# Optimization experiments

Measured on AMD Instinct MI355X. Metric: run time of the kernel, lower is better.

The kernel has to match this reference:

```python
import jax, jax.numpy as jnp
import numpy as np

B, NT, ND, NB = 2, 1024, 512, 6
K_IN, NH, K_LAT = 4 * NB + 5, 196, 128  # k_in = 2*NB*(1+1) + 2*(1+1) + 1 with USE_VELOCITIES=True
EPS_FREE = True  # norms divide exactly as in torch (no eps), randn inputs are safe


def setup_inputs() -> dict:
    key = jax.random.key(0)
    ks = jax.random.split(key, 12)
    def lin(k, fin, fout):
        kw, kb = jax.random.split(k)
        W = jax.random.normal(kw, (fin, fout), jnp.float32) / np.sqrt(fin)
        b = jax.random.normal(kb, (fout,), jnp.float32) * 0.01
        return W, b
    W0, b0 = lin(ks[0], K_IN, NH)
    W1, b1 = lin(ks[1], NH, NH)
    W2, b2 = lin(ks[2], NH, K_LAT)
    return {
        "x0": jax.random.normal(ks[3], (B, NT, 3), jnp.float32),
        "x": jax.random.normal(ks[4], (B, NT, ND, 3), jnp.float32),
        "N": jax.random.uniform(ks[5], (B, NT), jnp.float32),
        "basis": jax.random.normal(ks[6], (B, NB, 3), jnp.float32),
        "v": jax.random.normal(ks[7], (B, NT, ND, 3), jnp.float32),
        "W0": W0, "b0": b0, "W1": W1, "b1": b1, "W2": W2, "b2": b2,
    }


def _create_scalars(x0, x, N, basis, v):
    # shapes: x0 [b,i,3], x/v [b,i,j,3], N [b,i], basis [b,k,3]
    nd = x.shape[2]
    vbulk = jnp.mean(v, axis=2)                      # [b,i,3]
    vc = v - vbulk[:, :, None, :]                    # [b,i,j,3]

    bcast = lambda t: jnp.broadcast_to(t[:, :, None, :], t.shape[:2] + (nd, t.shape[-1]))

    x0n = jnp.linalg.norm(x0, axis=-1, keepdims=True)          # [b,i,1]
    x0b = jnp.einsum('bid,bkd->bik', x0 / x0n, basis)          # [b,i,NB]
    vbn = jnp.linalg.norm(vbulk, axis=-1, keepdims=True)       # [b,i,1]
    vbb = jnp.einsum('bid,bkd->bik', vbulk / vbn, basis)       # [b,i,NB]
    xn = jnp.linalg.norm(x, axis=-1, keepdims=True)            # [b,i,j,1]
    xb = jnp.einsum('bijd,bkd->bijk', x / xn, basis)           # [b,i,j,NB]
    vn = jnp.linalg.norm(vc, axis=-1, keepdims=True)           # [b,i,j,1]
    vb = jnp.einsum('bijd,bkd->bijk', vc / vn, basis)          # [b,i,j,NB]

    return jnp.concatenate([
        bcast(N[..., None]),   # N            [1]
        bcast(x0n),            # |x0|         [1]
        bcast(x0b),            # x0.basis     [NB]
        bcast(vbn),            # |vbulk|      [1]
        bcast(vbb),            # vbulk.basis  [NB]
        xn,                    # |x|          [1]
        xb,                    # x.basis      [NB]
        vn,                    # |v|          [1]
        vb,                    # v.basis      [NB]
    ], axis=-1)                # [b,i,j,K_IN]


def reference(x0, x, N, basis, v, W0, b0, W1, b1, W2, b2):
    s = _create_scalars(x0, x, N, basis, v)                    # [b,i,j,K_IN]
    h = jax.nn.leaky_relu(jnp.einsum('bijf,fh->bijh', s, W0) + b0)
    h = jnp.mean(h, axis=2)                                    # pool over N_DM -> [b,i,NH]
    h = jax.nn.leaky_relu(h @ W1 + b1)
    return h @ W2 + b2                                         # [b,i,K_LAT]
```

## Files before the change

### kernel.cpp

```cpp
#include <hip/hip_runtime.h>

typedef __bf16 bf16x8 __attribute__((ext_vector_type(8)));
typedef float f32x16 __attribute__((ext_vector_type(16)));

constexpr int NT = 1024;
constexpr int ND = 512;
constexpr int NB = 6;
constexpr int NH = 196;
constexpr int KL = 128;
constexpr int NHP = 224;

__device__ __forceinline__ unsigned short f2bf(float f) {
    unsigned int b = __float_as_uint(f);
    b += 0x7FFFu + ((b >> 16) & 1u);
    return (unsigned short)(b >> 16);
}

__global__ __launch_bounds__(448) void prep_kernel(const float* __restrict__ W0,
                                                   uint4* __restrict__ frag)
{
    const int tid = threadIdx.x;
    const int l = tid & 63;
    const int nt = tid >> 6;
    const int col = l & 31;
    const int khalf = l >> 5;
    const int c = nt * 32 + col;
    unsigned int w[4];
    #pragma unroll
    for (int d = 0; d < 4; d++) {
        int k0 = khalf * 8 + 2 * d;
        int k1 = k0 + 1;
        float v0 = (c < NH && k0 < 14) ? W0[(15 + k0) * NH + c] : 0.f;
        float v1 = (c < NH && k1 < 14) ? W0[(15 + k1) * NH + c] : 0.f;
        w[d] = (unsigned int)f2bf(v0) | ((unsigned int)f2bf(v1) << 16);
    }
    frag[tid] = make_uint4(w[0], w[1], w[2], w[3]);
}

__global__ __launch_bounds__(256) void pool_kernel(
    const float* __restrict__ x0, const float* __restrict__ x,
    const float* __restrict__ Nn, const float* __restrict__ basis,
    const float* __restrict__ v,  const float* __restrict__ W0,
    const float* __restrict__ b0, const uint4* __restrict__ w0frag,
    float* __restrict__ pool_out)
{
    __shared__ __align__(16) unsigned short featB[ND][16];
    __shared__ float consthL[NHP];
    __shared__ float pool4A[4][NHP];
    __shared__ float pool4B[4][NHP];
    __shared__ float red[4][3];

    const int r = blockIdx.x;
    const int t = threadIdx.x;
    const int wid = t >> 6;
    const int lane = t & 63;
    const int b = r >> 10;
    const size_t rowbase = (size_t)r * ND * 3;

    float s0 = 0.f, s1 = 0.f, s2 = 0.f;
    for (int j = t; j < ND; j += 256) {
        const float* vp = v + rowbase + 3 * j;
        s0 += vp[0]; s1 += vp[1]; s2 += vp[2];
    }
    #pragma unroll
    for (int off = 32; off > 0; off >>= 1) {
        s0 += __shfl_down(s0, off);
        s1 += __shfl_down(s1, off);
        s2 += __shfl_down(s2, off);
    }
    if (lane == 0) { red[wid][0] = s0; red[wid][1] = s1; red[wid][2] = s2; }
    __syncthreads();
    const float inv_nd = 1.0f / (float)ND;
    const float vb0 = (red[0][0] + red[1][0] + red[2][0] + red[3][0]) * inv_nd;
    const float vb1 = (red[0][1] + red[1][1] + red[2][1] + red[3][1]) * inv_nd;
    const float vb2 = (red[0][2] + red[1][2] + red[2][2] + red[3][2]) * inv_nd;

    float bx[NB], by[NB], bz[NB];
    {
        const float* bp = basis + (size_t)b * NB * 3;
        #pragma unroll
        for (int k = 0; k < NB; k++) { bx[k] = bp[3*k]; by[k] = bp[3*k+1]; bz[k] = bp[3*k+2]; }
    }

    for (int j = t; j < ND; j += 256) {
        const float* xp = x + rowbase + 3 * j;
        const float* vp = v + rowbase + 3 * j;
        float xa = xp[0], xbv = xp[1], xc = xp[2];
        float va = vp[0] - vb0, vbv = vp[1] - vb1, vcv = vp[2] - vb2;
        float n2x = xa*xa + xbv*xbv + xc*xc;
        float n2v = va*va + vbv*vbv + vcv*vcv;
        float rx = __frsqrt_rn(n2x);
        float rv = __frsqrt_rn(n2v);
        float f[14];
        f[0] = n2x * rx;
        #pragma unroll
        for (int k = 0; k < NB; k++) f[1+k] = (xa*bx[k] + xbv*by[k] + xc*bz[k]) * rx;
        f[7] = n2v * rv;
        #pragma unroll
        for (int k = 0; k < NB; k++) f[8+k] = (va*bx[k] + vbv*by[k] + vcv*bz[k]) * rv;
        bf16x8 lo, hi;
        #pragma unroll
        for (int e = 0; e < 8; e++) lo[e] = (__bf16)f[e];
        #pragma unroll
        for (int e = 0; e < 6; e++) hi[e] = (__bf16)f[8+e];
        hi[6] = (__bf16)0.f; hi[7] = (__bf16)0.f;
        *reinterpret_cast<uint4*>(&featB[j][0]) = __builtin_bit_cast(uint4, lo);
        *reinterpret_cast<uint4*>(&featB[j][8]) = __builtin_bit_cast(uint4, hi);
    }

    bf16x8 bfr[7];
    #pragma unroll
    for (int nt = 0; nt < 7; nt++)
        bfr[nt] = __builtin_bit_cast(bf16x8, w0frag[nt * 64 + lane]);

    float cf[15];
    {
        const float* xp = x0 + (size_t)r * 3;
        float a0 = xp[0], a1 = xp[1], a2 = xp[2];
        float n20 = a0*a0 + a1*a1 + a2*a2;
        float n2b = vb0*vb0 + vb1*vb1 + vb2*vb2;
        float r0 = __frsqrt_rn(n20);
        float r1 = __frsqrt_rn(n2b);
        cf[0] = Nn[r];
        cf[1] = n20 * r0;
        #pragma unroll
        for (int k = 0; k < NB; k++) cf[2+k] = (a0*bx[k] + a1*by[k] + a2*bz[k]) * r0;
        cf[8] = n2b * r1;
        #pragma unroll
        for (int k = 0; k < NB; k++) cf[9+k] = (vb0*bx[k] + vb1*by[k] + vb2*bz[k]) * r1;
    }
    if (t < NHP) {
        float ch = 0.f;
        if (t < NH) {
            ch = b0[t];
            #pragma unroll
            for (int f2 = 0; f2 < 15; f2++) ch += cf[f2] * W0[f2 * NH + t];
        }
        consthL[t] = ch;
    }
    __syncthreads();

    const int col = lane & 31;
    const int khalf = lane >> 5;
    float ch[7];
    #pragma unroll
    for (int nt = 0; nt < 7; nt++) ch[nt] = consthL[nt * 32 + col];

    float pA[7] = {0.f,0.f,0.f,0.f,0.f,0.f,0.f};
    float pB[7] = {0.f,0.f,0.f,0.f,0.f,0.f,0.f};
    #pragma unroll
    for (int mi = 0; mi < 4; mi++) {
        const int row = (wid * 4 + mi) * 32 + col;
        uint4 araw = *reinterpret_cast<const uint4*>(&featB[row][khalf * 8]);
        bf16x8 afrag = __builtin_bit_cast(bf16x8, araw);
        #pragma unroll
        for (int nt = 0; nt < 7; nt++) {
            f32x16 acc;
            #pragma unroll
            for (int i = 0; i < 16; i++) acc[i] = ch[nt];
            acc = __builtin_amdgcn_mfma_f32_32x32x16_bf16(afrag, bfr[nt], acc, 0, 0, 0);
            #pragma unroll
            for (int i = 0; i < 16; i++) {
                pA[nt] += acc[i];
                pB[nt] += __builtin_fabsf(acc[i]);
            }
        }
    }
    #pragma unroll
    for (int nt = 0; nt < 7; nt++) {
        pA[nt] += __shfl_xor(pA[nt], 32);
        pB[nt] += __shfl_xor(pB[nt], 32);
    }
    if (lane < 32) {
        #pragma unroll
        for (int nt = 0; nt < 7; nt++) {
            pool4A[wid][nt * 32 + lane] = pA[nt];
            pool4B[wid][nt * 32 + lane] = pB[nt];
        }
    }
    __syncthreads();

    if (t < NH) {
        float sa = pool4A[0][t] + pool4A[1][t] + pool4A[2][t] + pool4A[3][t];
        float sb = pool4B[0][t] + pool4B[1][t] + pool4B[2][t] + pool4B[3][t];
        pool_out[(size_t)r * NH + t] = (0.505f * sa + 0.495f * sb) * inv_nd;
    }
}

__global__ __launch_bounds__(256) void head_kernel(
    const float* __restrict__ pool, const float* __restrict__ W1,
    const float* __restrict__ b1,   const float* __restrict__ W2,
    const float* __restrict__ b2,   float* __restrict__ out)
{
    __shared__ __align__(16) float poolL[4][200];
    __shared__ __align__(16) float h1L[4][200];
    const int t = threadIdx.x;
    const int r0 = blockIdx.x * 4;

    if (t < NH) {
        #pragma unroll
        for (int rr = 0; rr < 4; rr++) poolL[rr][t] = pool[(size_t)(r0 + rr) * NH + t];
    }
    __syncthreads();

    if (t < NH) {
        float a0 = b1[t], a1 = b1[t], a2 = b1[t], a3 = b1[t];
        const float* wc = W1 + t;
        #pragma unroll 2
        for (int k = 0; k < NH; k += 4) {
            float w0 = wc[(size_t)(k + 0) * NH];
            float w1 = wc[(size_t)(k + 1) * NH];
            float w2 = wc[(size_t)(k + 2) * NH];
            float w3 = wc[(size_t)(k + 3) * NH];
            float4 p0 = *reinterpret_cast<const float4*>(&poolL[0][k]);
            float4 p1 = *reinterpret_cast<const float4*>(&poolL[1][k]);
            float4 p2 = *reinterpret_cast<const float4*>(&poolL[2][k]);
            float4 p3 = *reinterpret_cast<const float4*>(&poolL[3][k]);
            a0 += p0.x * w0 + p0.y * w1 + p0.z * w2 + p0.w * w3;
            a1 += p1.x * w0 + p1.y * w1 + p1.z * w2 + p1.w * w3;
            a2 += p2.x * w0 + p2.y * w1 + p2.z * w2 + p2.w * w3;
            a3 += p3.x * w0 + p3.y * w1 + p3.z * w2 + p3.w * w3;
        }
        h1L[0][t] = fmaxf(a0, 0.01f * a0);
        h1L[1][t] = fmaxf(a1, 0.01f * a1);
        h1L[2][t] = fmaxf(a2, 0.01f * a2);
        h1L[3][t] = fmaxf(a3, 0.01f * a3);
    }
    __syncthreads();

    if (t < KL) {
        float a0 = b2[t], a1 = b2[t], a2 = b2[t], a3 = b2[t];
        const float* wc = W2 + t;
        #pragma unroll 2
        for (int k = 0; k < NH; k += 4) {
            float w0 = wc[(size_t)(k + 0) * KL];
            float w1 = wc[(size_t)(k + 1) * KL];
            float w2 = wc[(size_t)(k + 2) * KL];
            float w3 = wc[(size_t)(k + 3) * KL];
            float4 p0 = *reinterpret_cast<const float4*>(&h1L[0][k]);
            float4 p1 = *reinterpret_cast<const float4*>(&h1L[1][k]);
            float4 p2 = *reinterpret_cast<const float4*>(&h1L[2][k]);
            float4 p3 = *reinterpret_cast<const float4*>(&h1L[3][k]);
            a0 += p0.x * w0 + p0.y * w1 + p0.z * w2 + p0.w * w3;
            a1 += p1.x * w0 + p1.y * w1 + p1.z * w2 + p1.w * w3;
            a2 += p2.x * w0 + p2.y * w1 + p2.z * w2 + p2.w * w3;
            a3 += p3.x * w0 + p3.y * w1 + p3.z * w2 + p3.w * w3;
        }
        out[(size_t)(r0 + 0) * KL + t] = a0;
        out[(size_t)(r0 + 1) * KL + t] = a1;
        out[(size_t)(r0 + 2) * KL + t] = a2;
        out[(size_t)(r0 + 3) * KL + t] = a3;
    }
}

extern "C" void kernel_launch(void* const* d_in, const int* in_sizes, int n_in,
                              void* d_out, int out_size, void* d_ws, size_t ws_size,
                              hipStream_t stream) {
    const float* x0    = (const float*)d_in[0];
    const float* x     = (const float*)d_in[1];
    const float* Nn    = (const float*)d_in[2];
    const float* basis = (const float*)d_in[3];
    const float* v     = (const float*)d_in[4];
    const float* W0    = (const float*)d_in[5];
    const float* b0    = (const float*)d_in[6];
    const float* W1    = (const float*)d_in[7];
    const float* b1    = (const float*)d_in[8];
    const float* W2    = (const float*)d_in[9];
    const float* b2    = (const float*)d_in[10];
    float* out = (float*)d_out;

    const int rows = in_sizes[2];
    float* pool_ws = (float*)d_ws;
    uint4* w0frag  = (uint4*)((char*)d_ws + (size_t)rows * NH * 4);

    prep_kernel<<<dim3(1), dim3(448), 0, stream>>>(W0, w0frag);
    pool_kernel<<<dim3(rows), dim3(256), 0, stream>>>(
        x0, x, Nn, basis, v, W0, b0, w0frag, pool_ws);
    head_kernel<<<dim3(rows / 4), dim3(256), 0, stream>>>(
        pool_ws, W1, b1, W2, b2, out);
}
```

Measured before the change: 151.4 us.

## Move head MLP layers to bf16 MFMA kernels with pre-packed weight fragments

```diff
diff --git a/kernel.cpp b/kernel.cpp
--- a/kernel.cpp
+++ b/kernel.cpp
@@ -9,6 +9,12 @@
 constexpr int NH = 196;
 constexpr int KL = 128;
 constexpr int NHP = 224;
+constexpr int KP = 208;
+
+constexpr size_t W0F_OFF = 0;
+constexpr size_t W1F_OFF = 7168;
+constexpr size_t W2F_OFF = 100352;
+constexpr size_t H1B_OFF = 153600;
 
 __device__ __forceinline__ unsigned short f2bf(float f) {
     unsigned int b = __float_as_uint(f);
@@ -16,25 +22,56 @@
     return (unsigned short)(b >> 16);
 }
 
-__global__ __launch_bounds__(448) void prep_kernel(const float* __restrict__ W0,
-                                                   uint4* __restrict__ frag)
+__global__ __launch_bounds__(256) void prep_kernel(
+    const float* __restrict__ W0, const float* __restrict__ W1,
+    const float* __restrict__ W2,
+    uint4* __restrict__ w0f, uint4* __restrict__ w1f, uint4* __restrict__ w2f)
 {
-    const int tid = threadIdx.x;
-    const int l = tid & 63;
-    const int nt = tid >> 6;
-    const int col = l & 31;
-    const int khalf = l >> 5;
-    const int c = nt * 32 + col;
-    unsigned int w[4];
-    #pragma unroll
-    for (int d = 0; d < 4; d++) {
-        int k0 = khalf * 8 + 2 * d;
-        int k1 = k0 + 1;
-        float v0 = (c < NH && k0 < 14) ? W0[(15 + k0) * NH + c] : 0.f;
-        float v1 = (c < NH && k1 < 14) ? W0[(15 + k1) * NH + c] : 0.f;
-        w[d] = (unsigned int)f2bf(v0) | ((unsigned int)f2bf(v1) << 16);
-    }
-    frag[tid] = make_uint4(w[0], w[1], w[2], w[3]);
+    const int tid = blockIdx.x * 256 + threadIdx.x;
+    if (tid < 448) {
+        const int l = tid & 63, nt = tid >> 6;
+        const int c = nt * 32 + (l & 31);
+        const int khalf = l >> 5;
+        unsigned int w[4];
+        #pragma unroll
+        for (int d = 0; d < 4; d++) {
+            int k0 = khalf * 8 + 2 * d, k1 = k0 + 1;
+            float v0 = (c < NH && k0 < 14) ? W0[(15 + k0) * NH + c] : 0.f;
+            float v1 = (c < NH && k1 < 14) ? W0[(15 + k1) * NH + c] : 0.f;
+            w[d] = (unsigned int)f2bf(v0) | ((unsigned int)f2bf(v1) << 16);
+        }
+        w0f[tid] = make_uint4(w[0], w[1], w[2], w[3]);
+    } else if (tid < 448 + 7 * 13 * 64) {
+        const int i = tid - 448;
+        const int l = i & 63, rest = i >> 6;
+        const int ks = rest % 13, nt = rest / 13;
+        const int c = nt * 32 + (l & 31);
+        const int kb = ks * 16 + (l >> 5) * 8;
+        unsigned int w[4];
+        #pragma unroll
+        for (int d = 0; d < 4; d++) {
+            int k0 = kb + 2 * d, k1 = k0 + 1;
+            float v0 = (c < NH && k0 < NH) ? W1[(size_t)k0 * NH + c] : 0.f;
+            float v1 = (c < NH && k1 < NH) ? W1[(size_t)k1 * NH + c] : 0.f;
+            w[d] = (unsigned int)f2bf(v0) | ((unsigned int)f2bf(v1) << 16);
+        }
+        w1f[i] = make_uint4(w[0], w[1], w[2], w[3]);
+    } else if (tid < 448 + 7 * 13 * 64 + 4 * 13 * 64) {
+        const int i = tid - 448 - 7 * 13 * 64;
+        const int l = i & 63, rest = i >> 6;
+        const int ks = rest % 13, nt = rest / 13;
+        const int c = nt * 32 + (l & 31);
+        const int kb = ks * 16 + (l >> 5) * 8;
+        unsigned int w[4];
+        #pragma unroll
+        for (int d = 0; d < 4; d++) {
+            int k0 = kb + 2 * d, k1 = k0 + 1;
+            float v0 = (k0 < NH) ? W2[(size_t)k0 * KL + c] : 0.f;
+            float v1 = (k1 < NH) ? W2[(size_t)k1 * KL + c] : 0.f;
+            w[d] = (unsigned int)f2bf(v0) | ((unsigned int)f2bf(v1) << 16);
+        }
+        w2f[i] = make_uint4(w[0], w[1], w[2], w[3]);
+    }
 }
 
 __global__ __launch_bounds__(256) void pool_kernel(
@@ -42,7 +79,7 @@
     const float* __restrict__ Nn, const float* __restrict__ basis,
     const float* __restrict__ v,  const float* __restrict__ W0,
     const float* __restrict__ b0, const uint4* __restrict__ w0frag,
-    float* __restrict__ pool_out)
+    unsigned short* __restrict__ pool_out)
 {
     __shared__ __align__(16) unsigned short featB[ND][16];
     __shared__ float consthL[NHP];
@@ -180,76 +217,78 @@
     }
     __syncthreads();
 
-    if (t < NH) {
-        float sa = pool4A[0][t] + pool4A[1][t] + pool4A[2][t] + pool4A[3][t];
-        float sb = pool4B[0][t] + pool4B[1][t] + pool4B[2][t] + pool4B[3][t];
-        pool_out[(size_t)r * NH + t] = (0.505f * sa + 0.495f * sb) * inv_nd;
-    }
-}
-
-__global__ __launch_bounds__(256) void head_kernel(
-    const float* __restrict__ pool, const float* __restrict__ W1,
-    const float* __restrict__ b1,   const float* __restrict__ W2,
-    const float* __restrict__ b2,   float* __restrict__ out)
+    if (t < KP) {
+        float val = 0.f;
+        if (t < NH) {
+            float sa = pool4A[0][t] + pool4A[1][t] + pool4A[2][t] + pool4A[3][t];
+            float sb = pool4B[0][t] + pool4B[1][t] + pool4B[2][t] + pool4B[3][t];
+            val = (0.505f * sa + 0.495f * sb) * inv_nd;
+        }
+        pool_out[(size_t)r * KP + t] = f2bf(val);
+    }
+}
+
+__global__ __launch_bounds__(64) void h1_kernel(
+    const unsigned short* __restrict__ poolb, const uint4* __restrict__ w1f,
+    const float* __restrict__ b1, unsigned short* __restrict__ h1b)
 {
-    __shared__ __align__(16) float poolL[4][200];
-    __shared__ __align__(16) float h1L[4][200];
-    const int t = threadIdx.x;
-    const int r0 = blockIdx.x * 4;
-
-    if (t < NH) {
-        #pragma unroll
-        for (int rr = 0; rr < 4; rr++) poolL[rr][t] = pool[(size_t)(r0 + rr) * NH + t];
-    }
-    __syncthreads();
-
-    if (t < NH) {
-        float a0 = b1[t], a1 = b1[t], a2 = b1[t], a3 = b1[t];
-        const float* wc = W1 + t;
-        #pragma unroll 2
-        for (int k = 0; k < NH; k += 4) {
-            float w0 = wc[(size_t)(k + 0) * NH];
-            float w1 = wc[(size_t)(k + 1) * NH];
-            float w2 = wc[(size_t)(k + 2) * NH];
-            float w3 = wc[(size_t)(k + 3) * NH];
-            float4 p0 = *reinterpret_cast<const float4*>(&poolL[0][k]);
-            float4 p1 = *reinterpret_cast<const float4*>(&poolL[1][k]);
-            float4 p2 = *reinterpret_cast<const float4*>(&poolL[2][k]);
-            float4 p3 = *reinterpret_cast<const float4*>(&poolL[3][k]);
-            a0 += p0.x * w0 + p0.y * w1 + p0.z * w2 + p0.w * w3;
-            a1 += p1.x * w0 + p1.y * w1 + p1.z * w2 + p1.w * w3;
-            a2 += p2.x * w0 + p2.y * w1 + p2.z * w2 + p2.w * w3;
-            a3 += p3.x * w0 + p3.y * w1 + p3.z * w2 + p3.w * w3;
-        }
-        h1L[0][t] = fmaxf(a0, 0.01f * a0);
-        h1L[1][t] = fmaxf(a1, 0.01f * a1);
-        h1L[2][t] = fmaxf(a2, 0.01f * a2);
-        h1L[3][t] = fmaxf(a3, 0.01f * a3);
-    }
-    __syncthreads();
-
-    if (t < KL) {
-        float a0 = b2[t], a1 = b2[t], a2 = b2[t], a3 = b2[t];
-        const float* wc = W2 + t;
-        #pragma unroll 2
-        for (int k = 0; k < NH; k += 4) {
-            float w0 = wc[(size_t)(k + 0) * KL];
-            float w1 = wc[(size_t)(k + 1) * KL];
-            float w2 = wc[(size_t)(k + 2) * KL];
-            float w3 = wc[(size_t)(k + 3) * KL];
-            float4 p0 = *reinterpret_cast<const float4*>(&h1L[0][k]);
-            float4 p1 = *reinterpret_cast<const float4*>(&h1L[1][k]);
-            float4 p2 = *reinterpret_cast<const float4*>(&h1L[2][k]);
-            float4 p3 = *reinterpret_cast<const float4*>(&h1L[3][k]);
-            a0 += p0.x * w0 + p0.y * w1 + p0.z * w2 + p0.w * w3;
-            a1 += p1.x * w0 + p1.y * w1 + p1.z * w2 + p1.w * w3;
-            a2 += p2.x * w0 + p2.y * w1 + p2.z * w2 + p2.w * w3;
-            a3 += p3.x * w0 + p3.y * w1 + p3.z * w2 + p3.w * w3;
-        }
-        out[(size_t)(r0 + 0) * KL + t] = a0;
-        out[(size_t)(r0 + 1) * KL + t] = a1;
-        out[(size_t)(r0 + 2) * KL + t] = a2;
-        out[(size_t)(r0 + 3) * KL + t] = a3;
+    const int rt = blockIdx.x / 7, nt = blockIdx.x % 7;
+    const int lane = threadIdx.x;
+    const int col = lane & 31, half = lane >> 5;
+    const int col_g = nt * 32 + col;
+
+    float binit = (col_g < NH) ? b1[col_g] : 0.f;
+    f32x16 acc;
+    #pragma unroll
+    for (int i = 0; i < 16; i++) acc[i] = binit;
+
+    const unsigned short* abase = poolb + (size_t)(rt * 32 + (lane & 31)) * KP + half * 8;
+    #pragma unroll
+    for (int ks = 0; ks < 13; ks++) {
+        uint4 a = *reinterpret_cast<const uint4*>(abase + ks * 16);
+        uint4 bq = w1f[(nt * 13 + ks) * 64 + lane];
+        acc = __builtin_amdgcn_mfma_f32_32x32x16_bf16(
+            __builtin_bit_cast(bf16x8, a), __builtin_bit_cast(bf16x8, bq), acc, 0, 0, 0);
+    }
+
+    if (col_g < KP) {
+        #pragma unroll
+        for (int i = 0; i < 16; i++) {
+            int row = (i & 3) + 8 * (i >> 2) + 4 * half;
+            float h = acc[i];
+            h = fmaxf(h, 0.01f * h);
+            h1b[(size_t)(rt * 32 + row) * KP + col_g] = f2bf(h);
+        }
+    }
+}
+
+__global__ __launch_bounds__(64) void h2_kernel(
+    const unsigned short* __restrict__ h1b, const uint4* __restrict__ w2f,
+    const float* __restrict__ b2, float* __restrict__ out)
+{
+    const int rt = blockIdx.x / 4, nt = blockIdx.x % 4;
+    const int lane = threadIdx.x;
+    const int col = lane & 31, half = lane >> 5;
+    const int col_g = nt * 32 + col;
+
+    float binit = b2[col_g];
+    f32x16 acc;
+    #pragma unroll
+    for (int i = 0; i < 16; i++) acc[i] = binit;
+
+    const unsigned short* abase = h1b + (size_t)(rt * 32 + (lane & 31)) * KP + half * 8;
+    #pragma unroll
+    for (int ks = 0; ks < 13; ks++) {
+        uint4 a = *reinterpret_cast<const uint4*>(abase + ks * 16);
+        uint4 bq = w2f[(nt * 13 + ks) * 64 + lane];
+        acc = __builtin_amdgcn_mfma_f32_32x32x16_bf16(
+            __builtin_bit_cast(bf16x8, a), __builtin_bit_cast(bf16x8, bq), acc, 0, 0, 0);
+    }
+
+    #pragma unroll
+    for (int i = 0; i < 16; i++) {
+        int row = (i & 3) + 8 * (i >> 2) + 4 * half;
+        out[(size_t)(rt * 32 + row) * KL + col_g] = acc[i];
     }
 }
 
@@ -269,13 +308,19 @@
     const float* b2    = (const float*)d_in[10];
     float* out = (float*)d_out;
 
+    char* ws = (char*)d_ws;
+    uint4* w0f = (uint4*)(ws + W0F_OFF);
+    uint4* w1f = (uint4*)(ws + W1F_OFF);
+    uint4* w2f = (uint4*)(ws + W2F_OFF);
+    unsigned short* h1b = (unsigned short*)(ws + H1B_OFF);
+    unsigned short* poolb = (unsigned short*)d_out;
+
     const int rows = in_sizes[2];
-    float* pool_ws = (float*)d_ws;
-    uint4* w0frag  = (uint4*)((char*)d_ws + (size_t)rows * NH * 4);
-
-    prep_kernel<<<dim3(1), dim3(448), 0, stream>>>(W0, w0frag);
+    const int prep_threads = 448 + 7 * 13 * 64 + 4 * 13 * 64;
+    prep_kernel<<<dim3((prep_threads + 255) / 256), dim3(256), 0, stream>>>(
+        W0, W1, W2, w0f, w1f, w2f);
     pool_kernel<<<dim3(rows), dim3(256), 0, stream>>>(
-        x0, x, Nn, basis, v, W0, b0, w0frag, pool_ws);
-    head_kernel<<<dim3(rows / 4), dim3(256), 0, stream>>>(
-        pool_ws, W1, b1, W2, b2, out);
-}
+        x0, x, Nn, basis, v, W0, b0, w0f, poolb);
+    h1_kernel<<<dim3((rows / 32) * 7), dim3(64), 0, stream>>>(poolb, w1f, b1, h1b);
+    h2_kernel<<<dim3((rows / 32) * 4), dim3(64), 0, stream>>>(h1b, w2f, b2, out);
+}
```

Result: faster. 129.5 us (-14.5%).
